# Kernel tuning notes

Measured on AMD Instinct MI355X. Metric: run time of the kernel, lower is better.

The kernel has to match this reference:

```python
import jax, jax.numpy as jnp
import numpy as np

B, S, T = 256, 2048, 64


def setup_inputs() -> dict:
    key = jax.random.key(0)
    k1, k2, k3, k4, k5 = jax.random.split(key, 5)
    emissions = jax.random.normal(k1, (B, S, T), dtype=jnp.float32)
    tags = jax.random.randint(k2, (B, S), 0, T)
    mask = jnp.ones((B, S), dtype=jnp.int32)
    start_transitions = jax.random.uniform(k3, (T,), minval=-1.0, maxval=1.0, dtype=jnp.float32)
    end_transitions = jax.random.uniform(k4, (T,), minval=-1.0, maxval=1.0, dtype=jnp.float32)
    transitions = jax.random.uniform(k5, (T, T), minval=-1.0, maxval=1.0, dtype=jnp.float32)
    return {
        'emissions': emissions,
        'start_transitions': start_transitions,
        'end_transitions': end_transitions,
        'transitions': transitions,
        'tags': tags,
        'mask': mask,
    }


def _crf_nll(emissions, start_transitions, end_transitions, transitions, tags, mask):
    # batch_first=True -> convert to time-major like the torch code
    em = jnp.swapaxes(emissions, 0, 1)            # (S, B, T)
    tg = tags.T                                   # (S, B)
    mk = mask.T.astype(emissions.dtype)           # (S, B)
    barange = jnp.arange(em.shape[1])

    # ---- numerator: score of the gold tag path ----
    score0 = start_transitions[tg[0]] + em[0, barange, tg[0]]  # (B,)

    def num_step(score, inp):
        em_i, tg_prev, tg_i, m_i = inp
        score = score + (transitions[tg_prev, tg_i] + em_i[barange, tg_i]) * m_i
        return score, None

    numerator, _ = jax.lax.scan(num_step, score0, (em[1:], tg[:-1], tg[1:], mk[1:]))
    seq_ends = mk.sum(axis=0).astype(jnp.int32) - 1            # (B,)
    last_tags = tg[seq_ends, barange]
    numerator = numerator + end_transitions[last_tags]

    # ---- denominator: log partition via forward algorithm (log-sum-exp semiring) ----
    alpha0 = start_transitions + em[0]                          # (B, T)

    def den_step(alpha, inp):
        em_i, m_i = inp
        # (B, T_prev, T_next) broadcast-add, reduce over T_prev
        nxt = jax.nn.logsumexp(alpha[:, :, None] + transitions[None, :, :] + em_i[:, None, :], axis=1)
        alpha = jnp.where(m_i[:, None] > 0, nxt, alpha)
        return alpha, None

    alpha, _ = jax.lax.scan(den_step, alpha0, (em[1:], mk[1:]))
    denominator = jax.nn.logsumexp(alpha + end_transitions, axis=1)  # (B,)

    return -(numerator - denominator).mean()


def reference(emissions, start_transitions, end_transitions, transitions, tags, mask):
    return _crf_nll(emissions, start_transitions, end_transitions, transitions, tags, mask)
```

## Files before the change

### kernel.cpp

```cpp
#include <hip/hip_runtime.h>

#define BB 256
#define SS 2048
#define TT 64
#define KC 32
#define LC 64
#define WARM 48
#define NSTEP (WARM + LC)
#define DEN_WAVES (BB * 2)
#define NSLOT 128
#define SLOT_STRIDE 32
#define LN2 0.69314718055994531f
#define LOG2E 1.4426950408889634f

typedef __fp16 half2v __attribute__((ext_vector_type(2)));
typedef __fp16 half8v __attribute__((ext_vector_type(8)));
typedef float float4v __attribute__((ext_vector_type(4)));

__device__ __forceinline__ float4v mfma16(half8v a, half8v b, float4v c) {
  return __builtin_amdgcn_mfma_f32_16x16x32_f16(a, b, c, 0, 0, 0);
}

__global__ __launch_bounds__(64) void crf_kernel(
    const float* __restrict__ em, const float* __restrict__ startT,
    const float* __restrict__ endT, const float* __restrict__ trans,
    const int* __restrict__ tags, const int* __restrict__ mask,
    float* __restrict__ acc, int slotmask) {
  const int lane = threadIdx.x;

  if (blockIdx.x >= DEN_WAVES) {
    const int b = blockIdx.x - DEN_WAVES;
    const int* tg = tags + b * SS;
    const int* mp = mask + b * SS;
    const float* emb = em + (size_t)b * SS * TT;
    float part = 0.f;
    int cnt = 0;
#pragma unroll 4
    for (int k = 0; k < SS / 64; ++k) {
      int i = k * 64 + lane;
      int m = mp[i];
      cnt += m;
      if (i >= 1 && m) {
        int t1 = tg[i], t0 = tg[i - 1];
        part += trans[t0 * TT + t1] + emb[(size_t)i * TT + t1];
      }
    }
#pragma unroll
    for (int o = 32; o > 0; o >>= 1) {
      part += __shfl_xor(part, o, 64);
      cnt += __shfl_xor(cnt, o, 64);
    }
    if (lane == 0) {
      int t0 = tg[0];
      float num = part + startT[t0] + emb[t0] + endT[tg[cnt - 1]];
      atomicAdd(acc + (size_t)(blockIdx.x & slotmask) * SLOT_STRIDE,
                -num * (1.0f / BB));
    }
    return;
  }

  const int b = blockIdx.x >> 1;
  const int hf = blockIdx.x & 1;
  const int s = lane & 15;
  const int g = lane >> 4;
  const int c = hf * 16 + s;
  const float* emB = em + (size_t)b * SS * TT;
  const size_t rowb = (size_t)b * SS;

  half8v A[4][2];
#pragma unroll
  for (int mt = 0; mt < 4; ++mt)
#pragma unroll
    for (int kt = 0; kt < 2; ++kt) {
      half8v f;
#pragma unroll
      for (int e = 0; e < 8; e += 2) {
        int k0 = 32 * kt + 16 * (e >> 2) + 4 * g + (e & 3);
        int m = 16 * mt + s;
        float v0 = __expf(trans[k0 * TT + m]) * 0.03125f;
        float v1 = __expf(trans[(k0 + 1) * TT + m]) * 0.03125f;
        half2v p = __builtin_amdgcn_cvt_pkrtz(v0, v1);
        f[e] = p[0];
        f[e + 1] = p[1];
      }
      A[mt][kt] = f;
    }

  half8v B0, B1;
#pragma unroll
  for (int e = 0; e < 8; ++e) {
    B0[e] = (__fp16)0.015625f;
    B1[e] = (__fp16)0.015625f;
  }
  float q0cur = 0.015625f;
  int esum = 0, nsteps = 0;
  float sS = 0.f, gamma = 0.f;
  float4v tf0, tf1, tf2, tf3;

  const int base = c * LC - WARM + 1;

  auto PF = [&](float4v(&buf)[4], int idx) {
    int p = base + idx;
    p = p < 0 ? 0 : (p > SS - 1 ? SS - 1 : p);
    const float* r = emB + (size_t)p * TT + 4 * g;
#pragma unroll
    for (int mt = 0; mt < 4; ++mt) buf[mt] = *(const float4v*)(r + 16 * mt);
  };
  auto EXP4 = [&](float4v v) {
    float4v r;
#pragma unroll
    for (int e = 0; e < 4; ++e) r[e] = __expf(v[e]);
    return r;
  };
  auto CORE = [&](float4v x0, float4v x1, float4v x2, float4v x3) {
    float4v z = {0.f, 0.f, 0.f, 0.f};
    tf0 = mfma16(A[0][0], B0, z);
    tf1 = mfma16(A[1][0], B0, z);
    tf2 = mfma16(A[2][0], B0, z);
    tf3 = mfma16(A[3][0], B0, z);
    tf0 = mfma16(A[0][1], B1, tf0);
    tf1 = mfma16(A[1][1], B1, tf1);
    tf2 = mfma16(A[2][1], B1, tf2);
    tf3 = mfma16(A[3][1], B1, tf3);
    tf0 *= x0; tf1 *= x1; tf2 *= x2; tf3 *= x3;
    float rv = __shfl(tf0[0], s, 64);
    int eb = __builtin_bit_cast(int, rv) & 0x7f800000;
    float sc = __builtin_bit_cast(float, 0x7C000000 - eb);
    esum += eb >> 23;
    nsteps += 1;
    q0cur = rv * sc;
    tf0 *= sc; tf1 *= sc; tf2 *= sc; tf3 *= sc;
    half2v p;
    p = __builtin_amdgcn_cvt_pkrtz(tf0[0], tf0[1]); B0[0] = p[0]; B0[1] = p[1];
    p = __builtin_amdgcn_cvt_pkrtz(tf0[2], tf0[3]); B0[2] = p[0]; B0[3] = p[1];
    p = __builtin_amdgcn_cvt_pkrtz(tf1[0], tf1[1]); B0[4] = p[0]; B0[5] = p[1];
    p = __builtin_amdgcn_cvt_pkrtz(tf1[2], tf1[3]); B0[6] = p[0]; B0[7] = p[1];
    p = __builtin_amdgcn_cvt_pkrtz(tf2[0], tf2[1]); B1[0] = p[0]; B1[1] = p[1];
    p = __builtin_amdgcn_cvt_pkrtz(tf2[2], tf2[3]); B1[2] = p[0]; B1[3] = p[1];
    p = __builtin_amdgcn_cvt_pkrtz(tf3[0], tf3[1]); B1[4] = p[0]; B1[5] = p[1];
    p = __builtin_amdgcn_cvt_pkrtz(tf3[2], tf3[3]); B1[6] = p[0]; B1[7] = p[1];
  };

  float4v bufA[4], bufB[4];
  PF(bufA, 0);
  PF(bufB, 1);

  for (int idx = 0; idx < 110; idx += 2) {
    if (idx == WARM) {
      sS = __log2f(q0cur) + (float)(6 + esum - 116 * nsteps);
      if (c == 0) {
        float aref = startT[0] + emB[0];
        gamma = aref * LOG2E;
        sS = 0.f;
        esum = 0;
        nsteps = 0;
        q0cur = 0.015625f;
#pragma unroll
        for (int e = 0; e < 8; ++e) {
          int t0i = 16 * (e >> 2) + 4 * g + (e & 3);
          B0[e] = (__fp16)(__expf(startT[t0i] + emB[t0i] - aref) * 0.015625f);
          B1[e] = (__fp16)(__expf(startT[t0i + 32] + emB[t0i + 32] - aref) *
                           0.015625f);
        }
      }
    }
    {
      float4v x0 = EXP4(bufA[0]), x1 = EXP4(bufA[1]), x2 = EXP4(bufA[2]),
              x3 = EXP4(bufA[3]);
      PF(bufA, idx + 2);
      CORE(x0, x1, x2, x3);
    }
    {
      float4v x0 = EXP4(bufB[0]), x1 = EXP4(bufB[1]), x2 = EXP4(bufB[2]),
              x3 = EXP4(bufB[3]);
      PF(bufB, idx + 3);
      CORE(x0, x1, x2, x3);
    }
  }
  {
    float4v x0 = EXP4(bufA[0]), x1 = EXP4(bufA[1]), x2 = EXP4(bufA[2]),
            x3 = EXP4(bufA[3]);
    CORE(x0, x1, x2, x3);
  }
  {
    half8v oB0 = B0, oB1 = B1;
    int oes = esum, on = nsteps;
    float oq = q0cur;
    float4v o0 = tf0, o1 = tf1, o2 = tf2, o3 = tf3;
    float4v x0 = EXP4(bufB[0]), x1 = EXP4(bufB[1]), x2 = EXP4(bufB[2]),
            x3 = EXP4(bufB[3]);
    CORE(x0, x1, x2, x3);
    int p = base + 111;
    int pc = p > SS - 1 ? SS - 1 : p;
    bool act = (p >= 1) && (p <= SS - 1) && (mask[rowb + pc] != 0);
    if (!act) {
      B0 = oB0; B1 = oB1; esum = oes; nsteps = on; q0cur = oq;
      tf0 = o0; tf1 = o1; tf2 = o2; tf3 = o3;
    }
  }

  float eS = __log2f(q0cur) + (float)(6 + esum - 116 * nsteps) + gamma;
  float contrib = LN2 * (eS - sS);

  float q0l = __log2f(q0cur);
  float4v ar0, ar1, ar2, ar3;
  float mx = -1e30f;
#pragma unroll
  for (int r = 0; r < 4; ++r) {
    ar0[r] = LN2 * (__log2f(tf0[r]) - q0l) + endT[4 * g + r];
    ar1[r] = LN2 * (__log2f(tf1[r]) - q0l) + endT[16 + 4 * g + r];
    ar2[r] = LN2 * (__log2f(tf2[r]) - q0l) + endT[32 + 4 * g + r];
    ar3[r] = LN2 * (__log2f(tf3[r]) - q0l) + endT[48 + 4 * g + r];
    mx = fmaxf(mx, fmaxf(fmaxf(ar0[r], ar1[r]), fmaxf(ar2[r], ar3[r])));
  }
  mx = fmaxf(mx, __shfl_xor(mx, 16, 64));
  mx = fmaxf(mx, __shfl_xor(mx, 32, 64));
  float ex = 0.f;
#pragma unroll
  for (int r = 0; r < 4; ++r)
    ex += __expf(ar0[r] - mx) + __expf(ar1[r] - mx) + __expf(ar2[r] - mx) +
          __expf(ar3[r] - mx);
  ex += __shfl_xor(ex, 16, 64);
  ex += __shfl_xor(ex, 32, 64);
  if (c == KC - 1) contrib += mx + __logf(ex);

  float val = (g == 0) ? contrib : 0.f;
#pragma unroll
  for (int o = 32; o > 0; o >>= 1) val += __shfl_xor(val, o, 64);
  if (lane == 0)
    atomicAdd(acc + (size_t)(blockIdx.x & slotmask) * SLOT_STRIDE,
              val * (1.0f / BB));
}

__global__ __launch_bounds__(64) void reduce_kernel(const float* __restrict__ ws,
                                                    float* __restrict__ out) {
  float v = ws[(size_t)threadIdx.x * SLOT_STRIDE] +
            ws[(size_t)(threadIdx.x + 64) * SLOT_STRIDE];
#pragma unroll
  for (int o = 32; o > 0; o >>= 1) v += __shfl_xor(v, o, 64);
  if (threadIdx.x == 0) *out = v;
}

extern "C" void kernel_launch(void* const* d_in, const int* in_sizes, int n_in,
                              void* d_out, int out_size, void* d_ws, size_t ws_size,
                              hipStream_t stream) {
  const float* em = (const float*)d_in[0];
  const float* startT = (const float*)d_in[1];
  const float* endT = (const float*)d_in[2];
  const float* trans = (const float*)d_in[3];
  const int* tags = (const int*)d_in[4];
  const int* mask = (const int*)d_in[5];
  float* out = (float*)d_out;

  const size_t need = (size_t)NSLOT * SLOT_STRIDE * sizeof(float);
  if (d_ws && ws_size >= need) {
    (void)hipMemsetAsync(d_ws, 0, need, stream);
    crf_kernel<<<DEN_WAVES + BB, 64, 0, stream>>>(em, startT, endT, trans, tags,
                                                  mask, (float*)d_ws, NSLOT - 1);
    reduce_kernel<<<1, 64, 0, stream>>>((const float*)d_ws, out);
  } else {
    (void)hipMemsetAsync(out, 0, sizeof(float), stream);
    crf_kernel<<<DEN_WAVES + BB, 64, 0, stream>>>(em, startT, endT, trans, tags,
                                                  mask, out, 0);
  }
}
```

Before: 237.6 us.

## Interleave two independent chunk recurrences per wave with shorter chunks

Each wave now advances two independent sequence chunks (64 chunks of 32 steps instead of 32 chunks of 64), interleaving their MFMA chains, shuffles and repacks. Interleaving is meant to hide the MFMA and shuffle dependency latency of the serial forward recurrence. Per-wave length becomes 32+48 warm-up steps instead of 64+48, but the warm-up overhead doubles relative to useful work and register pressure rises.

```diff
diff --git a/kernel.cpp b/kernel.cpp
--- a/kernel.cpp
+++ b/kernel.cpp
@@ -3,8 +3,8 @@
 #define BB 256
 #define SS 2048
 #define TT 64
-#define KC 32
-#define LC 64
+#define KC 64
+#define LC 32
 #define WARM 48
 #define NSTEP (WARM + LC)
 #define DEN_WAVES (BB * 2)
@@ -21,6 +21,81 @@
   return __builtin_amdgcn_mfma_f32_16x16x32_f16(a, b, c, 0, 0, 0);
 }
 
+struct GS {
+  half8v B0, B1;
+  float4v tf0, tf1, tf2, tf3;
+  float4v bufA[4], bufB[4];
+  float q0cur;
+  int esum, nsteps;
+  float sS, gamma;
+  int c, base;
+};
+
+__device__ __forceinline__ void pf(float4v (&buf)[4], const float* emB,
+                                   int base, int idx, int g) {
+  int p = base + idx;
+  p = p < 0 ? 0 : (p > SS - 1 ? SS - 1 : p);
+  const float* r = emB + (size_t)p * TT + 4 * g;
+#pragma unroll
+  for (int mt = 0; mt < 4; ++mt) buf[mt] = *(const float4v*)(r + 16 * mt);
+}
+
+__device__ __forceinline__ void exp4all(float4v (&x)[4], const float4v (&buf)[4]) {
+#pragma unroll
+  for (int mt = 0; mt < 4; ++mt)
+#pragma unroll
+    for (int e = 0; e < 4; ++e) x[mt][e] = __expf(buf[mt][e]);
+}
+
+__device__ __forceinline__ void repack(GS& a, float sc) {
+  a.tf0 *= sc; a.tf1 *= sc; a.tf2 *= sc; a.tf3 *= sc;
+  half2v p;
+  p = __builtin_amdgcn_cvt_pkrtz(a.tf0[0], a.tf0[1]); a.B0[0] = p[0]; a.B0[1] = p[1];
+  p = __builtin_amdgcn_cvt_pkrtz(a.tf0[2], a.tf0[3]); a.B0[2] = p[0]; a.B0[3] = p[1];
+  p = __builtin_amdgcn_cvt_pkrtz(a.tf1[0], a.tf1[1]); a.B0[4] = p[0]; a.B0[5] = p[1];
+  p = __builtin_amdgcn_cvt_pkrtz(a.tf1[2], a.tf1[3]); a.B0[6] = p[0]; a.B0[7] = p[1];
+  p = __builtin_amdgcn_cvt_pkrtz(a.tf2[0], a.tf2[1]); a.B1[0] = p[0]; a.B1[1] = p[1];
+  p = __builtin_amdgcn_cvt_pkrtz(a.tf2[2], a.tf2[3]); a.B1[2] = p[0]; a.B1[3] = p[1];
+  p = __builtin_amdgcn_cvt_pkrtz(a.tf3[0], a.tf3[1]); a.B1[4] = p[0]; a.B1[5] = p[1];
+  p = __builtin_amdgcn_cvt_pkrtz(a.tf3[2], a.tf3[3]); a.B1[6] = p[0]; a.B1[7] = p[1];
+}
+
+__device__ __forceinline__ void core2(const half8v (&A)[4][2], GS& a, GS& b,
+                                      const float4v (&xa)[4],
+                                      const float4v (&xb)[4], int s) {
+  const float4v z = {0.f, 0.f, 0.f, 0.f};
+  a.tf0 = mfma16(A[0][0], a.B0, z);
+  a.tf0 = mfma16(A[0][1], a.B1, a.tf0);
+  b.tf0 = mfma16(A[0][0], b.B0, z);
+  b.tf0 = mfma16(A[0][1], b.B1, b.tf0);
+  float rva = a.tf0[0] * xa[0][0];
+  float rvb = b.tf0[0] * xb[0][0];
+  float va = __shfl(rva, s, 64);
+  float vb = __shfl(rvb, s, 64);
+  a.tf1 = mfma16(A[1][0], a.B0, z);
+  a.tf1 = mfma16(A[1][1], a.B1, a.tf1);
+  b.tf1 = mfma16(A[1][0], b.B0, z);
+  b.tf1 = mfma16(A[1][1], b.B1, b.tf1);
+  a.tf2 = mfma16(A[2][0], a.B0, z);
+  a.tf2 = mfma16(A[2][1], a.B1, a.tf2);
+  b.tf2 = mfma16(A[2][0], b.B0, z);
+  b.tf2 = mfma16(A[2][1], b.B1, b.tf2);
+  a.tf3 = mfma16(A[3][0], a.B0, z);
+  a.tf3 = mfma16(A[3][1], a.B1, a.tf3);
+  b.tf3 = mfma16(A[3][0], b.B0, z);
+  b.tf3 = mfma16(A[3][1], b.B1, b.tf3);
+  a.tf0 *= xa[0]; a.tf1 *= xa[1]; a.tf2 *= xa[2]; a.tf3 *= xa[3];
+  b.tf0 *= xb[0]; b.tf1 *= xb[1]; b.tf2 *= xb[2]; b.tf3 *= xb[3];
+  int eba = __builtin_bit_cast(int, va) & 0x7f800000;
+  int ebb = __builtin_bit_cast(int, vb) & 0x7f800000;
+  float sca = __builtin_bit_cast(float, 0x7C000000 - eba);
+  float scb = __builtin_bit_cast(float, 0x7C000000 - ebb);
+  a.esum += eba >> 23; a.nsteps += 1; a.q0cur = va * sca;
+  b.esum += ebb >> 23; b.nsteps += 1; b.q0cur = vb * scb;
+  repack(a, sca);
+  repack(b, scb);
+}
+
 __global__ __launch_bounds__(64) void crf_kernel(
     const float* __restrict__ em, const float* __restrict__ startT,
     const float* __restrict__ endT, const float* __restrict__ trans,
@@ -29,10 +104,10 @@
   const int lane = threadIdx.x;
 
   if (blockIdx.x >= DEN_WAVES) {
-    const int b = blockIdx.x - DEN_WAVES;
-    const int* tg = tags + b * SS;
-    const int* mp = mask + b * SS;
-    const float* emb = em + (size_t)b * SS * TT;
+    const int bb = blockIdx.x - DEN_WAVES;
+    const int* tg = tags + bb * SS;
+    const int* mp = mask + bb * SS;
+    const float* emb = em + (size_t)bb * SS * TT;
     float part = 0.f;
     int cnt = 0;
 #pragma unroll 4
@@ -59,13 +134,12 @@
     return;
   }
 
-  const int b = blockIdx.x >> 1;
-  const int hf = blockIdx.x & 1;
+  const int bb = blockIdx.x >> 1;
+  const int h = blockIdx.x & 1;
   const int s = lane & 15;
   const int g = lane >> 4;
-  const int c = hf * 16 + s;
-  const float* emB = em + (size_t)b * SS * TT;
-  const size_t rowb = (size_t)b * SS;
+  const float* emB = em + (size_t)bb * SS * TT;
+  const size_t rowb = (size_t)bb * SS;
 
   half8v A[4][2];
 #pragma unroll
@@ -86,143 +160,122 @@
       A[mt][kt] = f;
     }
 
-  half8v B0, B1;
+  GS ga, gb;
+  ga.c = h * 32 + s;
+  gb.c = h * 32 + 16 + s;
+  ga.base = ga.c * LC - WARM + 1;
+  gb.base = gb.c * LC - WARM + 1;
 #pragma unroll
   for (int e = 0; e < 8; ++e) {
-    B0[e] = (__fp16)0.015625f;
-    B1[e] = (__fp16)0.015625f;
-  }
-  float q0cur = 0.015625f;
-  int esum = 0, nsteps = 0;
-  float sS = 0.f, gamma = 0.f;
-  float4v tf0, tf1, tf2, tf3;
-
-  const int base = c * LC - WARM + 1;
-
-  auto PF = [&](float4v(&buf)[4], int idx) {
-    int p = base + idx;
-    p = p < 0 ? 0 : (p > SS - 1 ? SS - 1 : p);
-    const float* r = emB + (size_t)p * TT + 4 * g;
-#pragma unroll
-    for (int mt = 0; mt < 4; ++mt) buf[mt] = *(const float4v*)(r + 16 * mt);
-  };
-  auto EXP4 = [&](float4v v) {
-    float4v r;
-#pragma unroll
-    for (int e = 0; e < 4; ++e) r[e] = __expf(v[e]);
-    return r;
-  };
-  auto CORE = [&](float4v x0, float4v x1, float4v x2, float4v x3) {
-    float4v z = {0.f, 0.f, 0.f, 0.f};
-    tf0 = mfma16(A[0][0], B0, z);
-    tf1 = mfma16(A[1][0], B0, z);
-    tf2 = mfma16(A[2][0], B0, z);
-    tf3 = mfma16(A[3][0], B0, z);
-    tf0 = mfma16(A[0][1], B1, tf0);
-    tf1 = mfma16(A[1][1], B1, tf1);
-    tf2 = mfma16(A[2][1], B1, tf2);
-    tf3 = mfma16(A[3][1], B1, tf3);
-    tf0 *= x0; tf1 *= x1; tf2 *= x2; tf3 *= x3;
-    float rv = __shfl(tf0[0], s, 64);
-    int eb = __builtin_bit_cast(int, rv) & 0x7f800000;
-    float sc = __builtin_bit_cast(float, 0x7C000000 - eb);
-    esum += eb >> 23;
-    nsteps += 1;
-    q0cur = rv * sc;
-    tf0 *= sc; tf1 *= sc; tf2 *= sc; tf3 *= sc;
-    half2v p;
-    p = __builtin_amdgcn_cvt_pkrtz(tf0[0], tf0[1]); B0[0] = p[0]; B0[1] = p[1];
-    p = __builtin_amdgcn_cvt_pkrtz(tf0[2], tf0[3]); B0[2] = p[0]; B0[3] = p[1];
-    p = __builtin_amdgcn_cvt_pkrtz(tf1[0], tf1[1]); B0[4] = p[0]; B0[5] = p[1];
-    p = __builtin_amdgcn_cvt_pkrtz(tf1[2], tf1[3]); B0[6] = p[0]; B0[7] = p[1];
-    p = __builtin_amdgcn_cvt_pkrtz(tf2[0], tf2[1]); B1[0] = p[0]; B1[1] = p[1];
-    p = __builtin_amdgcn_cvt_pkrtz(tf2[2], tf2[3]); B1[2] = p[0]; B1[3] = p[1];
-    p = __builtin_amdgcn_cvt_pkrtz(tf3[0], tf3[1]); B1[4] = p[0]; B1[5] = p[1];
-    p = __builtin_amdgcn_cvt_pkrtz(tf3[2], tf3[3]); B1[6] = p[0]; B1[7] = p[1];
-  };
-
-  float4v bufA[4], bufB[4];
-  PF(bufA, 0);
-  PF(bufB, 1);
-
-  for (int idx = 0; idx < 110; idx += 2) {
+    ga.B0[e] = (__fp16)0.015625f;
+    ga.B1[e] = (__fp16)0.015625f;
+    gb.B0[e] = (__fp16)0.015625f;
+    gb.B1[e] = (__fp16)0.015625f;
+  }
+  ga.q0cur = 0.015625f; ga.esum = 0; ga.nsteps = 0; ga.sS = 0.f; ga.gamma = 0.f;
+  gb.q0cur = 0.015625f; gb.esum = 0; gb.nsteps = 0; gb.sS = 0.f; gb.gamma = 0.f;
+
+  pf(ga.bufA, emB, ga.base, 0, g);
+  pf(gb.bufA, emB, gb.base, 0, g);
+  pf(ga.bufB, emB, ga.base, 1, g);
+  pf(gb.bufB, emB, gb.base, 1, g);
+
+  for (int idx = 0; idx < NSTEP - 2; idx += 2) {
     if (idx == WARM) {
-      sS = __log2f(q0cur) + (float)(6 + esum - 116 * nsteps);
-      if (c == 0) {
+      ga.sS = __log2f(ga.q0cur) + (float)(6 + ga.esum - 116 * ga.nsteps);
+      gb.sS = __log2f(gb.q0cur) + (float)(6 + gb.esum - 116 * gb.nsteps);
+      if (ga.c == 0) {
         float aref = startT[0] + emB[0];
-        gamma = aref * LOG2E;
-        sS = 0.f;
-        esum = 0;
-        nsteps = 0;
-        q0cur = 0.015625f;
+        ga.gamma = aref * LOG2E;
+        ga.sS = 0.f;
+        ga.esum = 0;
+        ga.nsteps = 0;
+        ga.q0cur = 0.015625f;
 #pragma unroll
         for (int e = 0; e < 8; ++e) {
           int t0i = 16 * (e >> 2) + 4 * g + (e & 3);
-          B0[e] = (__fp16)(__expf(startT[t0i] + emB[t0i] - aref) * 0.015625f);
-          B1[e] = (__fp16)(__expf(startT[t0i + 32] + emB[t0i + 32] - aref) *
-                           0.015625f);
+          ga.B0[e] = (__fp16)(__expf(startT[t0i] + emB[t0i] - aref) * 0.015625f);
+          ga.B1[e] = (__fp16)(__expf(startT[t0i + 32] + emB[t0i + 32] - aref) *
+                              0.015625f);
         }
       }
     }
     {
-      float4v x0 = EXP4(bufA[0]), x1 = EXP4(bufA[1]), x2 = EXP4(bufA[2]),
-              x3 = EXP4(bufA[3]);
-      PF(bufA, idx + 2);
-      CORE(x0, x1, x2, x3);
+      float4v xa[4], xb[4];
+      exp4all(xa, ga.bufA);
+      exp4all(xb, gb.bufA);
+      pf(ga.bufA, emB, ga.base, idx + 2, g);
+      pf(gb.bufA, emB, gb.base, idx + 2, g);
+      core2(A, ga, gb, xa, xb, s);
     }
     {
-      float4v x0 = EXP4(bufB[0]), x1 = EXP4(bufB[1]), x2 = EXP4(bufB[2]),
-              x3 = EXP4(bufB[3]);
-      PF(bufB, idx + 3);
-      CORE(x0, x1, x2, x3);
+      float4v xa[4], xb[4];
+      exp4all(xa, ga.bufB);
+      exp4all(xb, gb.bufB);
+      pf(ga.bufB, emB, ga.base, idx + 3, g);
+      pf(gb.bufB, emB, gb.base, idx + 3, g);
+      core2(A, ga, gb, xa, xb, s);
     }
   }
   {
-    float4v x0 = EXP4(bufA[0]), x1 = EXP4(bufA[1]), x2 = EXP4(bufA[2]),
-            x3 = EXP4(bufA[3]);
-    CORE(x0, x1, x2, x3);
+    float4v xa[4], xb[4];
+    exp4all(xa, ga.bufA);
+    exp4all(xb, gb.bufA);
+    core2(A, ga, gb, xa, xb, s);
   }
   {
-    half8v oB0 = B0, oB1 = B1;
-    int oes = esum, on = nsteps;
-    float oq = q0cur;
-    float4v o0 = tf0, o1 = tf1, o2 = tf2, o3 = tf3;
-    float4v x0 = EXP4(bufB[0]), x1 = EXP4(bufB[1]), x2 = EXP4(bufB[2]),
-            x3 = EXP4(bufB[3]);
-    CORE(x0, x1, x2, x3);
-    int p = base + 111;
-    int pc = p > SS - 1 ? SS - 1 : p;
-    bool act = (p >= 1) && (p <= SS - 1) && (mask[rowb + pc] != 0);
-    if (!act) {
-      B0 = oB0; B1 = oB1; esum = oes; nsteps = on; q0cur = oq;
-      tf0 = o0; tf1 = o1; tf2 = o2; tf3 = o3;
-    }
-  }
-
-  float eS = __log2f(q0cur) + (float)(6 + esum - 116 * nsteps) + gamma;
-  float contrib = LN2 * (eS - sS);
-
-  float q0l = __log2f(q0cur);
-  float4v ar0, ar1, ar2, ar3;
-  float mx = -1e30f;
-#pragma unroll
-  for (int r = 0; r < 4; ++r) {
-    ar0[r] = LN2 * (__log2f(tf0[r]) - q0l) + endT[4 * g + r];
-    ar1[r] = LN2 * (__log2f(tf1[r]) - q0l) + endT[16 + 4 * g + r];
-    ar2[r] = LN2 * (__log2f(tf2[r]) - q0l) + endT[32 + 4 * g + r];
-    ar3[r] = LN2 * (__log2f(tf3[r]) - q0l) + endT[48 + 4 * g + r];
-    mx = fmaxf(mx, fmaxf(fmaxf(ar0[r], ar1[r]), fmaxf(ar2[r], ar3[r])));
-  }
-  mx = fmaxf(mx, __shfl_xor(mx, 16, 64));
-  mx = fmaxf(mx, __shfl_xor(mx, 32, 64));
-  float ex = 0.f;
-#pragma unroll
-  for (int r = 0; r < 4; ++r)
-    ex += __expf(ar0[r] - mx) + __expf(ar1[r] - mx) + __expf(ar2[r] - mx) +
-          __expf(ar3[r] - mx);
-  ex += __shfl_xor(ex, 16, 64);
-  ex += __shfl_xor(ex, 32, 64);
-  if (c == KC - 1) contrib += mx + __logf(ex);
+    half8v oB0a = ga.B0, oB1a = ga.B1, oB0b = gb.B0, oB1b = gb.B1;
+    float4v o0a = ga.tf0, o1a = ga.tf1, o2a = ga.tf2, o3a = ga.tf3;
+    float4v o0b = gb.tf0, o1b = gb.tf1, o2b = gb.tf2, o3b = gb.tf3;
+    int oea = ga.esum, ona = ga.nsteps, oeb = gb.esum, onb = gb.nsteps;
+    float oqa = ga.q0cur, oqb = gb.q0cur;
+    float4v xa[4], xb[4];
+    exp4all(xa, ga.bufB);
+    exp4all(xb, gb.bufB);
+    core2(A, ga, gb, xa, xb, s);
+    int pa = ga.base + (NSTEP - 1);
+    int pca = pa > SS - 1 ? SS - 1 : pa;
+    bool acta = (pa >= 1) && (pa <= SS - 1) && (mask[rowb + pca] != 0);
+    if (!acta) {
+      ga.B0 = oB0a; ga.B1 = oB1a; ga.esum = oea; ga.nsteps = ona; ga.q0cur = oqa;
+      ga.tf0 = o0a; ga.tf1 = o1a; ga.tf2 = o2a; ga.tf3 = o3a;
+    }
+    int pb = gb.base + (NSTEP - 1);
+    int pcb = pb > SS - 1 ? SS - 1 : pb;
+    bool actb = (pb >= 1) && (pb <= SS - 1) && (mask[rowb + pcb] != 0);
+    if (!actb) {
+      gb.B0 = oB0b; gb.B1 = oB1b; gb.esum = oeb; gb.nsteps = onb; gb.q0cur = oqb;
+      gb.tf0 = o0b; gb.tf1 = o1b; gb.tf2 = o2b; gb.tf3 = o3b;
+    }
+  }
+
+  float eSa = __log2f(ga.q0cur) + (float)(6 + ga.esum - 116 * ga.nsteps) + ga.gamma;
+  float eSb = __log2f(gb.q0cur) + (float)(6 + gb.esum - 116 * gb.nsteps) + gb.gamma;
+  float contrib = LN2 * ((eSa - ga.sS) + (eSb - gb.sS));
+
+  {
+    float q0l = __log2f(gb.q0cur);
+    float4v ar0, ar1, ar2, ar3;
+    float mx = -1e30f;
+#pragma unroll
+    for (int r = 0; r < 4; ++r) {
+      ar0[r] = LN2 * (__log2f(gb.tf0[r]) - q0l) + endT[4 * g + r];
+      ar1[r] = LN2 * (__log2f(gb.tf1[r]) - q0l) + endT[16 + 4 * g + r];
+      ar2[r] = LN2 * (__log2f(gb.tf2[r]) - q0l) + endT[32 + 4 * g + r];
+      ar3[r] = LN2 * (__log2f(gb.tf3[r]) - q0l) + endT[48 + 4 * g + r];
+      mx = fmaxf(mx, fmaxf(fmaxf(ar0[r], ar1[r]), fmaxf(ar2[r], ar3[r])));
+    }
+    mx = fmaxf(mx, __shfl_xor(mx, 16, 64));
+    mx = fmaxf(mx, __shfl_xor(mx, 32, 64));
+    float ex = 0.f;
+#pragma unroll
+    for (int r = 0; r < 4; ++r)
+      ex += __expf(ar0[r] - mx) + __expf(ar1[r] - mx) + __expf(ar2[r] - mx) +
+            __expf(ar3[r] - mx);
+    ex += __shfl_xor(ex, 16, 64);
+    ex += __shfl_xor(ex, 32, 64);
+    if (gb.c == KC - 1) contrib += mx + __logf(ex);
+  }
 
   float val = (g == 0) ? contrib : 0.f;
 #pragma unroll
```

Measured after the change: 260.5 us. 9.6% more time.

## Split sequence into 64 chunks, deepen prefetch to 4 slots, reorder MFMA chain

Applied to the files above, without the earlier changes.

Halves the chunk length (LC 64→32) and doubles the chunk count so each batch row uses four waves instead of two, which shortens the serial forward-algorithm chain per wave (48 warmup + 32 steps instead of 112). The emission prefetch ring grows from two buffers to four. The MFMA order is changed so the first output tile and its shuffle for the renormalization scale are issued early, overlapping the shuffle with the remaining MFMAs. Wave-to-chunk mapping is interleaved across the grid. The trade-off is more redundant warmup work overall and more waves, plus more registers for the deeper buffer.

```diff
diff --git a/kernel.cpp b/kernel.cpp
--- a/kernel.cpp
+++ b/kernel.cpp
@@ -3,11 +3,11 @@
 #define BB 256
 #define SS 2048
 #define TT 64
-#define KC 32
-#define LC 64
+#define KC 64
+#define LC 32
 #define WARM 48
 #define NSTEP (WARM + LC)
-#define DEN_WAVES (BB * 2)
+#define DEN_WAVES (BB * 4)
 #define NSLOT 128
 #define SLOT_STRIDE 32
 #define LN2 0.69314718055994531f
@@ -29,10 +29,10 @@
   const int lane = threadIdx.x;
 
   if (blockIdx.x >= DEN_WAVES) {
-    const int b = blockIdx.x - DEN_WAVES;
-    const int* tg = tags + b * SS;
-    const int* mp = mask + b * SS;
-    const float* emb = em + (size_t)b * SS * TT;
+    const int bb = blockIdx.x - DEN_WAVES;
+    const int* tg = tags + bb * SS;
+    const int* mp = mask + bb * SS;
+    const float* emb = em + (size_t)bb * SS * TT;
     float part = 0.f;
     int cnt = 0;
 #pragma unroll 4
@@ -59,13 +59,15 @@
     return;
   }
 
-  const int b = blockIdx.x >> 1;
-  const int hf = blockIdx.x & 1;
+  const int w = blockIdx.x;
+  const int L = (w & 7) * (DEN_WAVES / 8) + (w >> 3);
+  const int bb = L >> 2;
+  const int quarter = L & 3;
   const int s = lane & 15;
   const int g = lane >> 4;
-  const int c = hf * 16 + s;
-  const float* emB = em + (size_t)b * SS * TT;
-  const size_t rowb = (size_t)b * SS;
+  const int c = quarter * 16 + s;
+  const float* emB = em + (size_t)bb * SS * TT;
+  const size_t rowb = (size_t)bb * SS;
 
   half8v A[4][2];
 #pragma unroll
@@ -99,36 +101,33 @@
 
   const int base = c * LC - WARM + 1;
 
-  auto PF = [&](float4v(&buf)[4], int idx) {
+  float4v buf[4][4];
+
+  auto PF = [&](int slot, int idx) {
     int p = base + idx;
     p = p < 0 ? 0 : (p > SS - 1 ? SS - 1 : p);
     const float* r = emB + (size_t)p * TT + 4 * g;
 #pragma unroll
-    for (int mt = 0; mt < 4; ++mt) buf[mt] = *(const float4v*)(r + 16 * mt);
+    for (int mt = 0; mt < 4; ++mt) buf[slot][mt] = *(const float4v*)(r + 16 * mt);
   };
-  auto EXP4 = [&](float4v v) {
-    float4v r;
-#pragma unroll
-    for (int e = 0; e < 4; ++e) r[e] = __expf(v[e]);
-    return r;
-  };
-  auto CORE = [&](float4v x0, float4v x1, float4v x2, float4v x3) {
-    float4v z = {0.f, 0.f, 0.f, 0.f};
+  auto CORE = [&](const float4v (&x)[4]) {
+    const float4v z = {0.f, 0.f, 0.f, 0.f};
     tf0 = mfma16(A[0][0], B0, z);
+    tf0 = mfma16(A[0][1], B1, tf0);
+    float rv = tf0[0] * x[0][0];
+    float v = __shfl(rv, s, 64);
     tf1 = mfma16(A[1][0], B0, z);
+    tf1 = mfma16(A[1][1], B1, tf1);
     tf2 = mfma16(A[2][0], B0, z);
+    tf2 = mfma16(A[2][1], B1, tf2);
     tf3 = mfma16(A[3][0], B0, z);
-    tf0 = mfma16(A[0][1], B1, tf0);
-    tf1 = mfma16(A[1][1], B1, tf1);
-    tf2 = mfma16(A[2][1], B1, tf2);
     tf3 = mfma16(A[3][1], B1, tf3);
-    tf0 *= x0; tf1 *= x1; tf2 *= x2; tf3 *= x3;
-    float rv = __shfl(tf0[0], s, 64);
-    int eb = __builtin_bit_cast(int, rv) & 0x7f800000;
+    tf0 *= x[0]; tf1 *= x[1]; tf2 *= x[2]; tf3 *= x[3];
+    int eb = __builtin_bit_cast(int, v) & 0x7f800000;
     float sc = __builtin_bit_cast(float, 0x7C000000 - eb);
     esum += eb >> 23;
     nsteps += 1;
-    q0cur = rv * sc;
+    q0cur = v * sc;
     tf0 *= sc; tf1 *= sc; tf2 *= sc; tf3 *= sc;
     half2v p;
     p = __builtin_amdgcn_cvt_pkrtz(tf0[0], tf0[1]); B0[0] = p[0]; B0[1] = p[1];
@@ -140,57 +139,55 @@
     p = __builtin_amdgcn_cvt_pkrtz(tf3[0], tf3[1]); B1[4] = p[0]; B1[5] = p[1];
     p = __builtin_amdgcn_cvt_pkrtz(tf3[2], tf3[3]); B1[6] = p[0]; B1[7] = p[1];
   };
-
-  float4v bufA[4], bufB[4];
-  PF(bufA, 0);
-  PF(bufB, 1);
-
-  for (int idx = 0; idx < 110; idx += 2) {
-    if (idx == WARM) {
-      sS = __log2f(q0cur) + (float)(6 + esum - 116 * nsteps);
-      if (c == 0) {
-        float aref = startT[0] + emB[0];
-        gamma = aref * LOG2E;
-        sS = 0.f;
-        esum = 0;
-        nsteps = 0;
-        q0cur = 0.015625f;
-#pragma unroll
-        for (int e = 0; e < 8; ++e) {
-          int t0i = 16 * (e >> 2) + 4 * g + (e & 3);
-          B0[e] = (__fp16)(__expf(startT[t0i] + emB[t0i] - aref) * 0.015625f);
-          B1[e] = (__fp16)(__expf(startT[t0i + 32] + emB[t0i + 32] - aref) *
-                           0.015625f);
-        }
-      }
-    }
-    {
-      float4v x0 = EXP4(bufA[0]), x1 = EXP4(bufA[1]), x2 = EXP4(bufA[2]),
-              x3 = EXP4(bufA[3]);
-      PF(bufA, idx + 2);
-      CORE(x0, x1, x2, x3);
-    }
-    {
-      float4v x0 = EXP4(bufB[0]), x1 = EXP4(bufB[1]), x2 = EXP4(bufB[2]),
-              x3 = EXP4(bufB[3]);
-      PF(bufB, idx + 3);
-      CORE(x0, x1, x2, x3);
-    }
-  }
-  {
-    float4v x0 = EXP4(bufA[0]), x1 = EXP4(bufA[1]), x2 = EXP4(bufA[2]),
-            x3 = EXP4(bufA[3]);
-    CORE(x0, x1, x2, x3);
-  }
+  auto STEP = [&](int slot, int pfIdx, bool doPf) {
+    float4v x[4];
+#pragma unroll
+    for (int mt = 0; mt < 4; ++mt)
+#pragma unroll
+      for (int e = 0; e < 4; ++e) x[mt][e] = __expf(buf[slot][mt][e]);
+    if (doPf) PF(slot, pfIdx);
+    CORE(x);
+  };
+
+#pragma unroll
+  for (int k = 0; k < 4; ++k) PF(k, k);
+
+  for (int idx = 0; idx < WARM; idx += 4) {
+#pragma unroll
+    for (int k = 0; k < 4; ++k) STEP(k, idx + k + 4, true);
+  }
+
+  sS = __log2f(q0cur) + (float)(6 + esum - 116 * nsteps);
+  if (c == 0) {
+    float aref = startT[0] + emB[0];
+    gamma = aref * LOG2E;
+    sS = 0.f;
+    esum = 0;
+    nsteps = 0;
+    q0cur = 0.015625f;
+#pragma unroll
+    for (int e = 0; e < 8; ++e) {
+      int t0i = 16 * (e >> 2) + 4 * g + (e & 3);
+      B0[e] = (__fp16)(__expf(startT[t0i] + emB[t0i] - aref) * 0.015625f);
+      B1[e] = (__fp16)(__expf(startT[t0i + 32] + emB[t0i + 32] - aref) *
+                       0.015625f);
+    }
+  }
+
+  for (int idx = WARM; idx < NSTEP - 4; idx += 4) {
+#pragma unroll
+    for (int k = 0; k < 4; ++k) STEP(k, idx + k + 4, true);
+  }
+  STEP(0, 0, false);
+  STEP(1, 0, false);
+  STEP(2, 0, false);
   {
     half8v oB0 = B0, oB1 = B1;
+    float4v o0 = tf0, o1 = tf1, o2 = tf2, o3 = tf3;
     int oes = esum, on = nsteps;
     float oq = q0cur;
-    float4v o0 = tf0, o1 = tf1, o2 = tf2, o3 = tf3;
-    float4v x0 = EXP4(bufB[0]), x1 = EXP4(bufB[1]), x2 = EXP4(bufB[2]),
-            x3 = EXP4(bufB[3]);
-    CORE(x0, x1, x2, x3);
-    int p = base + 111;
+    STEP(3, 0, false);
+    int p = base + (NSTEP - 1);
     int pc = p > SS - 1 ? SS - 1 : p;
     bool act = (p >= 1) && (p <= SS - 1) && (mask[rowb + pc] != 0);
     if (!act) {
@@ -202,27 +199,29 @@
   float eS = __log2f(q0cur) + (float)(6 + esum - 116 * nsteps) + gamma;
   float contrib = LN2 * (eS - sS);
 
-  float q0l = __log2f(q0cur);
-  float4v ar0, ar1, ar2, ar3;
-  float mx = -1e30f;
-#pragma unroll
-  for (int r = 0; r < 4; ++r) {
-    ar0[r] = LN2 * (__log2f(tf0[r]) - q0l) + endT[4 * g + r];
-    ar1[r] = LN2 * (__log2f(tf1[r]) - q0l) + endT[16 + 4 * g + r];
-    ar2[r] = LN2 * (__log2f(tf2[r]) - q0l) + endT[32 + 4 * g + r];
-    ar3[r] = LN2 * (__log2f(tf3[r]) - q0l) + endT[48 + 4 * g + r];
-    mx = fmaxf(mx, fmaxf(fmaxf(ar0[r], ar1[r]), fmaxf(ar2[r], ar3[r])));
-  }
-  mx = fmaxf(mx, __shfl_xor(mx, 16, 64));
-  mx = fmaxf(mx, __shfl_xor(mx, 32, 64));
-  float ex = 0.f;
-#pragma unroll
-  for (int r = 0; r < 4; ++r)
-    ex += __expf(ar0[r] - mx) + __expf(ar1[r] - mx) + __expf(ar2[r] - mx) +
-          __expf(ar3[r] - mx);
-  ex += __shfl_xor(ex, 16, 64);
-  ex += __shfl_xor(ex, 32, 64);
-  if (c == KC - 1) contrib += mx + __logf(ex);
+  {
+    float q0l = __log2f(q0cur);
+    float4v ar0, ar1, ar2, ar3;
+    float mx = -1e30f;
+#pragma unroll
+    for (int r = 0; r < 4; ++r) {
+      ar0[r] = LN2 * (__log2f(tf0[r]) - q0l) + endT[4 * g + r];
+      ar1[r] = LN2 * (__log2f(tf1[r]) - q0l) + endT[16 + 4 * g + r];
+      ar2[r] = LN2 * (__log2f(tf2[r]) - q0l) + endT[32 + 4 * g + r];
+      ar3[r] = LN2 * (__log2f(tf3[r]) - q0l) + endT[48 + 4 * g + r];
+      mx = fmaxf(mx, fmaxf(fmaxf(ar0[r], ar1[r]), fmaxf(ar2[r], ar3[r])));
+    }
+    mx = fmaxf(mx, __shfl_xor(mx, 16, 64));
+    mx = fmaxf(mx, __shfl_xor(mx, 32, 64));
+    float ex = 0.f;
+#pragma unroll
+    for (int r = 0; r < 4; ++r)
+      ex += __expf(ar0[r] - mx) + __expf(ar1[r] - mx) + __expf(ar2[r] - mx) +
+            __expf(ar3[r] - mx);
+    ex += __shfl_xor(ex, 16, 64);
+    ex += __shfl_xor(ex, 32, 64);
+    if (c == KC - 1) contrib += mx + __logf(ex);
+  }
 
   float val = (g == 0) ? contrib : 0.f;
 #pragma unroll
```

Result: slower. 252.8 us (+6.4%).
